# Optimization experiments

Hardware: AMD Instinct MI355X
Metric: run time of the kernel (lower is better)

Reference implementation:

```python
import jax, jax.numpy as jnp
import numpy as np

B, C, IMG, P, D, L, NH, DFF = 8, 2, 256, 16, 1024, 8, 16, 4096
HP = IMG // P          # 16 patches per side
N = HP * HP            # 256 patch tokens
S = N + 1              # + cls token
HD = D // NH           # 64 head dim


def _ln(x, w, b, eps=1e-5):
    mu = x.mean(-1, keepdims=True)
    var = ((x - mu) ** 2).mean(-1, keepdims=True)
    return (x - mu) * jax.lax.rsqrt(var + eps) * w + b


def _decay_mask():
    # RetNetRelPos2d(D, NH, initial_value=1, heads_range=NH): per-head log-decay
    decay = jnp.log(1.0 - 2.0 ** (-1.0 - NH * jnp.arange(NH, dtype=jnp.float32) / NH))
    idx = jnp.arange(HP)
    gy, gx = jnp.meshgrid(idx, idx, indexing='ij')
    grid = jnp.stack([gy.ravel(), gx.ravel()], -1)                 # [N,2]
    dist = jnp.abs(grid[:, None] - grid[None, :]).sum(-1)          # [N,N] Manhattan
    mask = decay[:, None, None] * dist.astype(jnp.float32)        # [NH,N,N]
    return jnp.pad(mask, ((0, 0), (1, 0), (1, 0)))                 # cls: zero decay


def setup_inputs() -> dict:
    key = jax.random.key(0)
    ks = iter(jax.random.split(key, 16))
    g = lambda shape: jax.random.normal(next(ks), shape, jnp.float32) * 0.02
    return dict(
        imgs=jax.random.normal(next(ks), (B, C, IMG, IMG), jnp.float32),
        patch_w=g((C, P, P, D)), patch_b=jnp.zeros((D,), jnp.float32),
        cls_tok=g((1, 1, D)),
        ln1_w=jnp.ones((L, D), jnp.float32), ln1_b=jnp.zeros((L, D), jnp.float32),
        wq=g((L, D, D)), wk=g((L, D, D)), wv=g((L, D, D)),
        bq=jnp.zeros((L, D), jnp.float32), bk=jnp.zeros((L, D), jnp.float32), bv=jnp.zeros((L, D), jnp.float32),
        wo=g((L, D, D)), bo=jnp.zeros((L, D), jnp.float32),
        ln2_w=jnp.ones((L, D), jnp.float32), ln2_b=jnp.zeros((L, D), jnp.float32),
        w1=g((L, D, DFF)), b1=jnp.zeros((L, DFF), jnp.float32),
        w2=g((L, DFF, D)), b2=jnp.zeros((L, D), jnp.float32),
        normf_w=jnp.ones((D,), jnp.float32), normf_b=jnp.zeros((D,), jnp.float32),
        enpred_w=g((D, P * P * 2)), enpred_b=jnp.zeros((P * P * 2,), jnp.float32),
    )


def reference(imgs, patch_w, patch_b, cls_tok, ln1_w, ln1_b, wq, wk, wv, bq, bk, bv,
              wo, bo, ln2_w, ln2_b, w1, b1, w2, b2, normf_w, normf_b, enpred_w, enpred_b):
    b = imgs.shape[0]
    # PatchEmbed: conv with stride==kernel == patch extraction + linear
    xp = imgs.reshape(b, C, HP, P, HP, P)
    x = jnp.einsum('nchpwq,cpqd->nhwd', xp, patch_w).reshape(b, N, D) + patch_b
    residual = x
    x = jnp.concatenate([jnp.broadcast_to(cls_tok, (b, 1, D)), x], axis=1)  # [b,S,D]
    mask = _decay_mask()  # [NH,S,S]
    scale = HD ** -0.5
    for i in range(L):  # RMT blocks: pre-LN MaSA (softmax(qk*scale + decay)) + pre-LN GELU MLP
        h = _ln(x, ln1_w[i], ln1_b[i])
        q = (h @ wq[i] + bq[i]).reshape(b, S, NH, HD)
        k = (h @ wk[i] + bk[i]).reshape(b, S, NH, HD)
        v = (h @ wv[i] + bv[i]).reshape(b, S, NH, HD)
        logits = jnp.einsum('bqhd,bkhd->bhqk', q, k) * scale + mask
        attn = jax.nn.softmax(logits, axis=-1)
        o = jnp.einsum('bhqk,bkhd->bqhd', attn, v).reshape(b, S, D)
        x = x + o @ wo[i] + bo[i]
        h = _ln(x, ln2_w[i], ln2_b[i])
        x = x + jax.nn.gelu(h @ w1[i] + b1[i], approximate=False) @ w2[i] + b2[i]
    x = _ln(x, normf_w, normf_b)
    # PGSA on patch tokens as [b,D,HP,HP]
    t = x[:, 1:, :].transpose(0, 2, 1).reshape(b, D, HP, HP)
    n = HP * HP - 1
    mu = t.mean(axis=(2, 3), keepdims=True)
    xm2 = (t - mu) ** 2
    y = xm2 / (4.0 * (xm2.sum(axis=(2, 3), keepdims=True) / n + 1e-4)) + 0.5
    t = t * jax.nn.sigmoid(y)
    tokens = t.reshape(b, D, N).transpose(0, 2, 1) + residual
    pred = tokens @ enpred_w + enpred_b  # [b,N,P*P*2]
    # unpatchify -> [b,2,IMG,IMG]
    u = pred.reshape(b, HP, HP, P, P, 2)
    return jnp.einsum('nhwpqc->nchpwq', u).reshape(b, 2, IMG, IMG)
```

## Files before the change

### kernel.cpp

```cpp
#include <hip/hip_runtime.h>
#include <cstdint>
#include <cstddef>

#define BB    8
#define CCH   2
#define IMGD  256
#define PDIM  16
#define DD    1024
#define LLAY  8
#define NHEAD 16
#define DFFD  4096
#define NTOK  256
#define SD    257
#define HDD   64
#define MTOK  (BB*SD)
#define MPAT  (BB*NTOK)
#define MPAD  2176
#define KPAD  288

typedef unsigned short u16;
typedef __bf16 bf16x8 __attribute__((ext_vector_type(8)));
typedef float  f32x4  __attribute__((ext_vector_type(4)));

__device__ __forceinline__ u16 f2bf(float f) {
    uint32_t u = __float_as_uint(f);
    u += 0x7FFF + ((u >> 16) & 1);
    return (u16)(u >> 16);
}
__device__ __forceinline__ int imin(int a, int b) { return a < b ? a : b; }

#define GLB(p)  ((const __attribute__((address_space(1))) void*)(uintptr_t)(p))
#define LDSP(p) ((__attribute__((address_space(3))) void*)(uint32_t)(uintptr_t)(p))

template<int ACT, int OBF>
__global__ __launch_bounds__(256) void gemm128(
    const u16* __restrict__ A, const u16* __restrict__ BT,
    const float* __restrict__ bias, const float* __restrict__ Cin,
    void* __restrict__ Cout, int M, int N, int K)
{
    __shared__ u16 lds[8192];
    const int tid = threadIdx.x, wid = tid >> 6, lane = tid & 63;
    const int m0 = blockIdx.y * 128, n0 = blockIdx.x * 128;
    const int wm = (wid >> 1) * 64, wn = (wid & 1) * 64;
    const int srow = lane >> 2, scol = (lane & 3) * 8;
    const int l15 = lane & 15, loct = lane >> 4;

    f32x4 acc[4][4] = {};

    const size_t arow = (size_t)(m0 + wid * 16 + srow) * K + scol;
    const size_t brow = (size_t)(n0 + wid * 16 + srow) * K + scol;
    u16* ldsA = lds + wid * 512;
    u16* ldsB = lds + 4096 + wid * 512;

    for (int k0 = 0; k0 < K; k0 += 32) {
        __builtin_amdgcn_global_load_lds(GLB(A  + arow + k0),                 LDSP(ldsA),        16, 0, 0);
        __builtin_amdgcn_global_load_lds(GLB(A  + arow + (size_t)64*K + k0),  LDSP(ldsA + 2048), 16, 0, 0);
        __builtin_amdgcn_global_load_lds(GLB(BT + brow + k0),                 LDSP(ldsB),        16, 0, 0);
        __builtin_amdgcn_global_load_lds(GLB(BT + brow + (size_t)64*K + k0),  LDSP(ldsB + 2048), 16, 0, 0);
        __syncthreads();
        bf16x8 af[4], bfr[4];
        #pragma unroll
        for (int i = 0; i < 4; ++i)
            af[i] = *(const bf16x8*)(lds + (wm + i * 16 + l15) * 32 + loct * 8);
        #pragma unroll
        for (int j = 0; j < 4; ++j)
            bfr[j] = *(const bf16x8*)(lds + 4096 + (wn + j * 16 + l15) * 32 + loct * 8);
        #pragma unroll
        for (int i = 0; i < 4; ++i)
            #pragma unroll
            for (int j = 0; j < 4; ++j)
                acc[i][j] = __builtin_amdgcn_mfma_f32_16x16x32_bf16(af[i], bfr[j], acc[i][j], 0, 0, 0);
        __syncthreads();
    }

    #pragma unroll
    for (int j = 0; j < 4; ++j) {
        const int col = n0 + wn + j * 16 + l15;
        const float bv = bias[col];
        #pragma unroll
        for (int i = 0; i < 4; ++i) {
            const int rbase = m0 + wm + i * 16 + loct * 4;
            #pragma unroll
            for (int r = 0; r < 4; ++r) {
                const int row = rbase + r;
                if (row < M) {
                    float v = acc[i][j][r] + bv;
                    if (ACT) v = 0.5f * v * (1.f + erff(v * 0.70710678118654752f));
                    if (Cin) v += Cin[(size_t)row * N + col];
                    if (OBF) ((u16*)Cout)[(size_t)row * N + col] = f2bf(v);
                    else     ((float*)Cout)[(size_t)row * N + col] = v;
                }
            }
        }
    }
}

template<int SPLIT>
__global__ __launch_bounds__(256) void gemm128_sk(
    const u16* __restrict__ A, const u16* __restrict__ BT,
    const float* __restrict__ bias, float* __restrict__ C,
    int M, int N, int K)
{
    __shared__ u16 lds[8192];
    const int tid = threadIdx.x, wid = tid >> 6, lane = tid & 63;
    const int m0 = blockIdx.y * 128, n0 = blockIdx.x * 128;
    const int wm = (wid >> 1) * 64, wn = (wid & 1) * 64;
    const int srow = lane >> 2, scol = (lane & 3) * 8;
    const int l15 = lane & 15, loct = lane >> 4;
    const int Ks = K / SPLIT;
    const int kb = blockIdx.z * Ks;

    f32x4 acc[4][4] = {};

    const size_t arow = (size_t)(m0 + wid * 16 + srow) * K + scol + kb;
    const size_t brow = (size_t)(n0 + wid * 16 + srow) * K + scol + kb;
    u16* ldsA = lds + wid * 512;
    u16* ldsB = lds + 4096 + wid * 512;

    for (int k0 = 0; k0 < Ks; k0 += 32) {
        __builtin_amdgcn_global_load_lds(GLB(A  + arow + k0),                 LDSP(ldsA),        16, 0, 0);
        __builtin_amdgcn_global_load_lds(GLB(A  + arow + (size_t)64*K + k0),  LDSP(ldsA + 2048), 16, 0, 0);
        __builtin_amdgcn_global_load_lds(GLB(BT + brow + k0),                 LDSP(ldsB),        16, 0, 0);
        __builtin_amdgcn_global_load_lds(GLB(BT + brow + (size_t)64*K + k0),  LDSP(ldsB + 2048), 16, 0, 0);
        __syncthreads();
        bf16x8 af[4], bfr[4];
        #pragma unroll
        for (int i = 0; i < 4; ++i)
            af[i] = *(const bf16x8*)(lds + (wm + i * 16 + l15) * 32 + loct * 8);
        #pragma unroll
        for (int j = 0; j < 4; ++j)
            bfr[j] = *(const bf16x8*)(lds + 4096 + (wn + j * 16 + l15) * 32 + loct * 8);
        #pragma unroll
        for (int i = 0; i < 4; ++i)
            #pragma unroll
            for (int j = 0; j < 4; ++j)
                acc[i][j] = __builtin_amdgcn_mfma_f32_16x16x32_bf16(af[i], bfr[j], acc[i][j], 0, 0, 0);
        __syncthreads();
    }

    const int z0 = (blockIdx.z == 0);
    #pragma unroll
    for (int j = 0; j < 4; ++j) {
        const int col = n0 + wn + j * 16 + l15;
        const float bv = z0 ? bias[col] : 0.f;
        #pragma unroll
        for (int i = 0; i < 4; ++i) {
            const int rbase = m0 + wm + i * 16 + loct * 4;
            #pragma unroll
            for (int r = 0; r < 4; ++r) {
                const int row = rbase + r;
                if (row < M)
                    unsafeAtomicAdd(&C[(size_t)row * N + col], acc[i][j][r] + bv);
            }
        }
    }
}

__global__ __launch_bounds__(256) void gemm_qkv(
    const u16* __restrict__ A, const u16* __restrict__ BT,
    const float* __restrict__ bq, const float* __restrict__ bk,
    const float* __restrict__ bvp,
    u16* __restrict__ QKb, u16* __restrict__ VTg, int M, int K)
{
    __shared__ u16 lds[8192];
    const int tid = threadIdx.x, wid = tid >> 6, lane = tid & 63;
    const int m0 = blockIdx.y * 128, n0 = blockIdx.x * 128;
    const int wm = (wid >> 1) * 64, wn = (wid & 1) * 64;
    const int srow = lane >> 2, scol = (lane & 3) * 8;
    const int l15 = lane & 15, loct = lane >> 4;

    f32x4 acc[4][4] = {};
    const size_t arow = (size_t)(m0 + wid * 16 + srow) * K + scol;
    const size_t brow = (size_t)(n0 + wid * 16 + srow) * K + scol;
    u16* ldsA = lds + wid * 512;
    u16* ldsB = lds + 4096 + wid * 512;

    for (int k0 = 0; k0 < K; k0 += 32) {
        __builtin_amdgcn_global_load_lds(GLB(A  + arow + k0),                 LDSP(ldsA),        16, 0, 0);
        __builtin_amdgcn_global_load_lds(GLB(A  + arow + (size_t)64*K + k0),  LDSP(ldsA + 2048), 16, 0, 0);
        __builtin_amdgcn_global_load_lds(GLB(BT + brow + k0),                 LDSP(ldsB),        16, 0, 0);
        __builtin_amdgcn_global_load_lds(GLB(BT + brow + (size_t)64*K + k0),  LDSP(ldsB + 2048), 16, 0, 0);
        __syncthreads();
        bf16x8 af[4], bfr[4];
        #pragma unroll
        for (int i = 0; i < 4; ++i)
            af[i] = *(const bf16x8*)(lds + (wm + i * 16 + l15) * 32 + loct * 8);
        #pragma unroll
        for (int j = 0; j < 4; ++j)
            bfr[j] = *(const bf16x8*)(lds + 4096 + (wn + j * 16 + l15) * 32 + loct * 8);
        #pragma unroll
        for (int i = 0; i < 4; ++i)
            #pragma unroll
            for (int j = 0; j < 4; ++j)
                acc[i][j] = __builtin_amdgcn_mfma_f32_16x16x32_bf16(af[i], bfr[j], acc[i][j], 0, 0, 0);
        __syncthreads();
    }

    #pragma unroll
    for (int j = 0; j < 4; ++j) {
        const int col = n0 + wn + j * 16 + l15;
        const float bval = (col < 1024) ? bq[col]
                         : (col < 2048) ? bk[col - 1024]
                                        : bvp[col - 2048];
        #pragma unroll
        for (int i = 0; i < 4; ++i) {
            const int rbase = m0 + wm + i * 16 + loct * 4;
            #pragma unroll
            for (int r = 0; r < 4; ++r) {
                const int row = rbase + r;
                if (row < M) {
                    const float v = acc[i][j][r] + bval;
                    if (col < 2048) {
                        QKb[(size_t)row * 2048 + col] = f2bf(v);
                    } else {
                        const int b = row / SD;
                        const int key = row - b * SD;
                        VTg[((size_t)b * 1024 + (col - 2048)) * KPAD + key] = f2bf(v);
                    }
                }
            }
        }
    }
}

template<int ACT, int OBF>
__global__ __launch_bounds__(256) void gemm64(
    const u16* __restrict__ A, const u16* __restrict__ BT,
    const float* __restrict__ bias, const float* __restrict__ Cin,
    void* __restrict__ Cout, int M, int N, int K)
{
    __shared__ u16 lds[8192];
    const int tid = threadIdx.x, wid = tid >> 6, lane = tid & 63;
    const int m0 = blockIdx.y * 64, n0 = blockIdx.x * 64;
    const int wm = (wid >> 1) * 32, wn = (wid & 1) * 32;
    const int srow = lane >> 2, scol = (lane & 3) * 8;
    const int l15 = lane & 15, loct = lane >> 4;

    f32x4 acc[2][2] = {};
    const size_t arow = (size_t)(m0 + wid * 16 + srow) * K + scol;
    const size_t brow = (size_t)(n0 + wid * 16 + srow) * K + scol;
    u16* ldsA = lds + wid * 512;
    u16* ldsB = lds + 4096 + wid * 512;

    for (int k0 = 0; k0 < K; k0 += 64) {
        __builtin_amdgcn_global_load_lds(GLB(A  + arow + k0),      LDSP(ldsA),        16, 0, 0);
        __builtin_amdgcn_global_load_lds(GLB(A  + arow + k0 + 32), LDSP(ldsA + 2048), 16, 0, 0);
        __builtin_amdgcn_global_load_lds(GLB(BT + brow + k0),      LDSP(ldsB),        16, 0, 0);
        __builtin_amdgcn_global_load_lds(GLB(BT + brow + k0 + 32), LDSP(ldsB + 2048), 16, 0, 0);
        __syncthreads();
        #pragma unroll
        for (int t = 0; t < 2; ++t) {
            bf16x8 af[2], bfr[2];
            #pragma unroll
            for (int i = 0; i < 2; ++i)
                af[i] = *(const bf16x8*)(lds + t * 2048 + (wm + i * 16 + l15) * 32 + loct * 8);
            #pragma unroll
            for (int j = 0; j < 2; ++j)
                bfr[j] = *(const bf16x8*)(lds + 4096 + t * 2048 + (wn + j * 16 + l15) * 32 + loct * 8);
            #pragma unroll
            for (int i = 0; i < 2; ++i)
                #pragma unroll
                for (int j = 0; j < 2; ++j)
                    acc[i][j] = __builtin_amdgcn_mfma_f32_16x16x32_bf16(af[i], bfr[j], acc[i][j], 0, 0, 0);
        }
        __syncthreads();
    }

    #pragma unroll
    for (int j = 0; j < 2; ++j) {
        const int col = n0 + wn + j * 16 + l15;
        const float bv = bias[col];
        #pragma unroll
        for (int i = 0; i < 2; ++i) {
            const int rbase = m0 + wm + i * 16 + loct * 4;
            #pragma unroll
            for (int r = 0; r < 4; ++r) {
                const int row = rbase + r;
                if (row < M) {
                    float v = acc[i][j][r] + bv;
                    if (ACT) v = 0.5f * v * (1.f + erff(v * 0.70710678118654752f));
                    if (Cin) v += Cin[(size_t)row * N + col];
                    if (OBF) ((u16*)Cout)[(size_t)row * N + col] = f2bf(v);
                    else     ((float*)Cout)[(size_t)row * N + col] = v;
                }
            }
        }
    }
}

__global__ __launch_bounds__(256) void attn_fused(
    const u16* __restrict__ QKb, const u16* __restrict__ VTg,
    u16* __restrict__ O)
{
    __shared__ u16 P[4][16][296];
    const int tid = threadIdx.x, wid = tid >> 6, lane = tid & 63;
    const int l15 = lane & 15, loct = lane >> 4;
    const int bh = blockIdx.x, b = bh >> 4, h = bh & 15;
    const int q0 = blockIdx.y * 64 + wid * 16;

    const size_t qkbase = (size_t)b * SD * 2048 + h * 64;
    const u16* qp = QKb + qkbase + (size_t)imin(q0 + l15, SD - 1) * 2048;
    const bf16x8 qf0 = *(const bf16x8*)(qp + loct * 8);
    const bf16x8 qf1 = *(const bf16x8*)(qp + 32 + loct * 8);

    f32x4 s[17];
    #pragma unroll
    for (int nt = 0; nt < 17; ++nt) {
        const u16* kp = QKb + qkbase + (size_t)imin(nt * 16 + l15, SD - 1) * 2048 + 1024;
        const bf16x8 kf0 = *(const bf16x8*)(kp + loct * 8);
        const bf16x8 kf1 = *(const bf16x8*)(kp + 32 + loct * 8);
        f32x4 a = {};
        a = __builtin_amdgcn_mfma_f32_16x16x32_bf16(qf0, kf0, a, 0, 0, 0);
        a = __builtin_amdgcn_mfma_f32_16x16x32_bf16(qf1, kf1, a, 0, 0, 0);
        s[nt] = a;
    }

    const float dec = logf(1.f - exp2f(-1.f - (float)h));
    const int qb = q0 + loct * 4;
    float rmax[4] = {-3.4e38f, -3.4e38f, -3.4e38f, -3.4e38f};
    #pragma unroll
    for (int nt = 0; nt < 17; ++nt) {
        const int key = nt * 16 + l15;
        #pragma unroll
        for (int r = 0; r < 4; ++r) {
            float v;
            if (key >= SD) {
                v = -1e30f;
            } else {
                v = s[nt][r] * 0.125f;
                const int q = qb + r;
                if (q > 0 && key > 0) {
                    const int nq = q - 1, nk = key - 1;
                    const int dist = abs((nq >> 4) - (nk >> 4)) + abs((nq & 15) - (nk & 15));
                    v += dec * (float)dist;
                }
            }
            s[nt][r] = v;
            rmax[r] = fmaxf(rmax[r], v);
        }
    }
    #pragma unroll
    for (int r = 0; r < 4; ++r) {
        #pragma unroll
        for (int m = 1; m < 16; m <<= 1) rmax[r] = fmaxf(rmax[r], __shfl_xor(rmax[r], m));
    }
    float rsum[4] = {0.f, 0.f, 0.f, 0.f};
    #pragma unroll
    for (int nt = 0; nt < 17; ++nt)
        #pragma unroll
        for (int r = 0; r < 4; ++r) {
            const float e = __expf(s[nt][r] - rmax[r]);
            s[nt][r] = e;
            rsum[r] += e;
        }
    #pragma unroll
    for (int r = 0; r < 4; ++r) {
        #pragma unroll
        for (int m = 1; m < 16; m <<= 1) rsum[r] += __shfl_xor(rsum[r], m);
        rsum[r] = 1.f / rsum[r];
    }
    #pragma unroll
    for (int nt = 0; nt < 17; ++nt)
        #pragma unroll
        for (int r = 0; r < 4; ++r)
            P[wid][loct * 4 + r][nt * 16 + l15] = f2bf(s[nt][r] * rsum[r]);
    {
        const int rr = lane >> 2, cc = (lane & 3) * 4;
        #pragma unroll
        for (int i = 0; i < 4; ++i) P[wid][rr][272 + cc + i] = 0;
    }

    f32x4 o[4] = {};
    const u16* vrow = VTg + ((size_t)b * 1024 + h * 64) * KPAD;
    #pragma unroll
    for (int ks = 0; ks < 9; ++ks) {
        const bf16x8 pf = *(const bf16x8*)&P[wid][l15][ks * 32 + loct * 8];
        #pragma unroll
        for (int j = 0; j < 4; ++j) {
            const bf16x8 vf = *(const bf16x8*)(vrow + (size_t)(j * 16 + l15) * KPAD + ks * 32 + loct * 8);
            o[j] = __builtin_amdgcn_mfma_f32_16x16x32_bf16(pf, vf, o[j], 0, 0, 0);
        }
    }
    #pragma unroll
    for (int j = 0; j < 4; ++j)
        #pragma unroll
        for (int r = 0; r < 4; ++r) {
            const int q = qb + r;
            if (q < SD) O[((size_t)(b * SD + q)) * DD + h * 64 + j * 16 + l15] = f2bf(o[j][r]);
        }
}

__global__ __launch_bounds__(256) void transpose_bf16_b(
    const float* __restrict__ W, u16* __restrict__ WT, int K, int N,
    size_t sstrideZ, size_t dstrideZ)
{
    __shared__ float t[32][33];
    const float* Wz = W + (size_t)blockIdx.z * sstrideZ;
    u16* WTz = WT + (size_t)blockIdx.z * dstrideZ;
    const int k0 = blockIdx.y * 32, n0 = blockIdx.x * 32;
    const int c = threadIdx.x & 31, rb = threadIdx.x >> 5;
    #pragma unroll
    for (int i = 0; i < 4; ++i) {
        const int r = rb + i * 8;
        t[r][c] = Wz[(size_t)(k0 + r) * N + n0 + c];
    }
    __syncthreads();
    #pragma unroll
    for (int i = 0; i < 4; ++i) {
        const int r = rb + i * 8;
        WTz[(size_t)(n0 + r) * K + k0 + c] = f2bf(t[c][r]);
    }
}

__global__ __launch_bounds__(256) void im2col_k(const float* __restrict__ imgs,
                                                u16* __restrict__ Ao)
{
    const int idx = blockIdx.x * 256 + threadIdx.x;
    const int k = idx & 511, m = idx >> 9;
    const int b = m >> 8, n = m & 255;
    const int hp = n >> 4, wp = n & 15;
    const int c = k >> 8, p = (k >> 4) & 15, q = k & 15;
    Ao[idx] = f2bf(imgs[(((size_t)b * CCH + c) * IMGD + hp * PDIM + p) * IMGD + wp * PDIM + q]);
}

__global__ __launch_bounds__(256) void build_x_k(const float* __restrict__ RES,
                                                 const float* __restrict__ cls,
                                                 float* __restrict__ X)
{
    const int idx = blockIdx.x * 256 + threadIdx.x;
    const int d = idx & 1023;
    const int r = idx >> 10;
    const int b = r / SD;
    const int s = r - b * SD;
    X[idx] = (s == 0) ? cls[d] : RES[((size_t)(b * NTOK + s - 1)) * DD + d];
}

template<int OBF>
__global__ __launch_bounds__(256) void ln_rows(const float* __restrict__ X,
                                               const float* __restrict__ w,
                                               const float* __restrict__ bsrc,
                                               void* __restrict__ Y)
{
    const int row = blockIdx.x;
    const int tid = threadIdx.x;
    const float* xr = X + (size_t)row * DD;
    const float4 v = *(const float4*)(xr + tid * 4);
    float s  = v.x + v.y + v.z + v.w;
    float s2 = v.x * v.x + v.y * v.y + v.z * v.z + v.w * v.w;
    #pragma unroll
    for (int off = 1; off < 64; off <<= 1) {
        s  += __shfl_xor(s, off);
        s2 += __shfl_xor(s2, off);
    }
    __shared__ float rs[4], rs2[4];
    if ((tid & 63) == 0) { rs[tid >> 6] = s; rs2[tid >> 6] = s2; }
    __syncthreads();
    s  = rs[0] + rs[1] + rs[2] + rs[3];
    s2 = rs2[0] + rs2[1] + rs2[2] + rs2[3];
    const float mu  = s * (1.f / 1024.f);
    const float var = fmaf(-mu, mu, s2 * (1.f / 1024.f));
    const float ri  = rsqrtf(var + 1e-5f);
    const float4 wv = *(const float4*)(w + tid * 4);
    const float4 bv = *(const float4*)(bsrc + tid * 4);
    float4 o;
    o.x = (v.x - mu) * ri * wv.x + bv.x;
    o.y = (v.y - mu) * ri * wv.y + bv.y;
    o.z = (v.z - mu) * ri * wv.z + bv.z;
    o.w = (v.w - mu) * ri * wv.w + bv.w;
    if (OBF) {
        ushort4 o4 = make_ushort4(f2bf(o.x), f2bf(o.y), f2bf(o.z), f2bf(o.w));
        *(ushort4*)((u16*)Y + (size_t)row * DD + tid * 4) = o4;
    } else {
        *(float4*)((float*)Y + (size_t)row * DD + tid * 4) = o;
    }
}

__global__ __launch_bounds__(256) void pgsa_k(const float* __restrict__ Xf,
                                              const float* __restrict__ RES,
                                              u16* __restrict__ TOK)
{
    const int bd = blockIdx.x;
    const int b = bd >> 10, dch = bd & 1023;
    const int n = threadIdx.x;
    const float t = Xf[((size_t)(b * SD + 1 + n)) * DD + dch];
    __shared__ float red[4];
    float s = t;
    #pragma unroll
    for (int off = 1; off < 64; off <<= 1) s += __shfl_xor(s, off);
    if ((n & 63) == 0) red[n >> 6] = s;
    __syncthreads();
    const float mu = (red[0] + red[1] + red[2] + red[3]) * (1.f / 256.f);
    const float xm = t - mu;
    const float xm2 = xm * xm;
    __syncthreads();
    float s2 = xm2;
    #pragma unroll
    for (int off = 1; off < 64; off <<= 1) s2 += __shfl_xor(s2, off);
    if ((n & 63) == 0) red[n >> 6] = s2;
    __syncthreads();
    const float tot2 = red[0] + red[1] + red[2] + red[3];
    const float y = xm2 / (4.f * (tot2 * (1.f / 255.f) + 1e-4f)) + 0.5f;
    const float sig = 1.f / (1.f + expf(-y));
    const size_t ri = ((size_t)b * NTOK + n) * DD + dch;
    TOK[ri] = f2bf(fmaf(t, sig, RES[ri]));
}

__global__ __launch_bounds__(256) void unpatch_k(const float* __restrict__ PRED,
                                                 float* __restrict__ out)
{
    const int idx = blockIdx.x * 256 + threadIdx.x;
    const int j = idx & 255, i = (idx >> 8) & 255;
    const int c = (idx >> 16) & 1, b = idx >> 17;
    const int hp = i >> 4, p = i & 15, wp = j >> 4, q = j & 15;
    out[idx] = PRED[((size_t)b * NTOK + hp * 16 + wp) * 512 + (p * 16 + q) * 2 + c];
}

extern "C" void kernel_launch(void* const* d_in, const int* in_sizes, int n_in,
                              void* d_out, int out_size, void* d_ws, size_t ws_size,
                              hipStream_t stream)
{
    const float* imgs     = (const float*)d_in[0];
    const float* patch_w  = (const float*)d_in[1];
    const float* patch_b  = (const float*)d_in[2];
    const float* cls_tok  = (const float*)d_in[3];
    const float* ln1_w    = (const float*)d_in[4];
    const float* ln1_b    = (const float*)d_in[5];
    const float* wq       = (const float*)d_in[6];
    const float* wk       = (const float*)d_in[7];
    const float* wv       = (const float*)d_in[8];
    const float* bq       = (const float*)d_in[9];
    const float* bk       = (const float*)d_in[10];
    const float* bv       = (const float*)d_in[11];
    const float* wo       = (const float*)d_in[12];
    const float* bo       = (const float*)d_in[13];
    const float* ln2_w    = (const float*)d_in[14];
    const float* ln2_b    = (const float*)d_in[15];
    const float* w1       = (const float*)d_in[16];
    const float* b1       = (const float*)d_in[17];
    const float* w2       = (const float*)d_in[18];
    const float* b2       = (const float*)d_in[19];
    const float* normf_w  = (const float*)d_in[20];
    const float* normf_b  = (const float*)d_in[21];
    const float* enpred_w = (const float*)d_in[22];
    const float* enpred_b = (const float*)d_in[23];
    float* out = (float*)d_out;

    char* w = (char*)d_ws;
    float* X     = (float*)w;            w += (size_t)MTOK * DD * 4;
    float* RES   = (float*)w;            w += (size_t)MPAT * DD * 4;
    u16*   QKb   = (u16*)w;              w += (size_t)MPAD * 2048 * 2;
    u16*   VTg   = (u16*)w;              w += (size_t)BB * 1024 * KPAD * 2;
    char*  UNION = w;                    w += (size_t)MPAD * DFFD * 2;
    u16*   Hb    = (u16*)w;              w += (size_t)MPAD * DD * 2;
    u16*   Ob    = (u16*)w;              w += (size_t)MPAD * DD * 2;
    u16*   WTqkv = (u16*)w;              w += (size_t)LLAY * 3072 * DD * 2;
    u16*   WTwo  = (u16*)w;              w += (size_t)LLAY * DD * DD * 2;
    u16*   WTw1  = (u16*)w;              w += (size_t)LLAY * DFFD * DD * 2;
    u16*   WTw2  = (u16*)w;              w += (size_t)LLAY * DD * DFFD * 2;
    u16*   WTpe  = (u16*)w;              w += (size_t)DD * 512 * 2;
    u16*   WTen  = (u16*)w;              w += (size_t)512 * DD * 2;

    u16*   IM2b  = (u16*)UNION;
    u16*   GELUb = (u16*)UNION;
    float* PRED  = (float*)UNION;
    float* Hf    = (float*)QKb;
    u16*   TOKb  = Hb;

    hipMemsetAsync(VTg, 0, (size_t)BB * 1024 * KPAD * 2, stream);

    hipLaunchKernelGGL(transpose_bf16_b, dim3(DD / 32, 512 / 32, 1), dim3(256), 0, stream,
                       patch_w, WTpe, 512, DD, 0, 0);
    hipLaunchKernelGGL(transpose_bf16_b, dim3(32, 32, LLAY), dim3(256), 0, stream,
                       wq, WTqkv,                     DD, DD, (size_t)DD * DD, (size_t)3072 * DD);
    hipLaunchKernelGGL(transpose_bf16_b, dim3(32, 32, LLAY), dim3(256), 0, stream,
                       wk, WTqkv + (size_t)1024 * DD, DD, DD, (size_t)DD * DD, (size_t)3072 * DD);
    hipLaunchKernelGGL(transpose_bf16_b, dim3(32, 32, LLAY), dim3(256), 0, stream,
                       wv, WTqkv + (size_t)2048 * DD, DD, DD, (size_t)DD * DD, (size_t)3072 * DD);
    hipLaunchKernelGGL(transpose_bf16_b, dim3(32, 32, LLAY), dim3(256), 0, stream,
                       wo, WTwo, DD, DD, (size_t)DD * DD, (size_t)DD * DD);
    hipLaunchKernelGGL(transpose_bf16_b, dim3(DFFD / 32, DD / 32, LLAY), dim3(256), 0, stream,
                       w1, WTw1, DD, DFFD, (size_t)DD * DFFD, (size_t)DFFD * DD);
    hipLaunchKernelGGL(transpose_bf16_b, dim3(DD / 32, DFFD / 32, LLAY), dim3(256), 0, stream,
                       w2, WTw2, DFFD, DD, (size_t)DFFD * DD, (size_t)DD * DFFD);
    hipLaunchKernelGGL(transpose_bf16_b, dim3(512 / 32, DD / 32, 1), dim3(256), 0, stream,
                       enpred_w, WTen, DD, 512, 0, 0);

    hipLaunchKernelGGL(im2col_k, dim3(4096), dim3(256), 0, stream, imgs, IM2b);
    hipLaunchKernelGGL((gemm64<0,0>), dim3(DD / 64, MPAT / 64), dim3(256), 0, stream,
                       IM2b, WTpe, patch_b, (const float*)nullptr, (void*)RES, MPAT, DD, 512);
    hipLaunchKernelGGL(build_x_k, dim3(MTOK * DD / 256), dim3(256), 0, stream, RES, cls_tok, X);

    for (int i = 0; i < LLAY; ++i) {
        hipLaunchKernelGGL((ln_rows<1>), dim3(MTOK), dim3(256), 0, stream,
                           X, ln1_w + i * DD, ln1_b + i * DD, (void*)Hb);
        hipLaunchKernelGGL(gemm_qkv, dim3(3072 / 128, 17), dim3(256), 0, stream,
                           Hb, WTqkv + (size_t)i * 3072 * DD,
                           bq + i * DD, bk + i * DD, bv + i * DD, QKb, VTg, MTOK, DD);
        hipLaunchKernelGGL(attn_fused, dim3(BB * NHEAD, 5), dim3(256), 0, stream,
                           QKb, VTg, Ob);
        hipLaunchKernelGGL((gemm64<0,0>), dim3(DD / 64, 33), dim3(256), 0, stream,
                           Ob, WTwo + (size_t)i * DD * DD, bo + i * DD, X, (void*)X, MTOK, DD, DD);
        hipLaunchKernelGGL((ln_rows<1>), dim3(MTOK), dim3(256), 0, stream,
                           X, ln2_w + i * DD, ln2_b + i * DD, (void*)Hb);
        hipLaunchKernelGGL((gemm128<1,1>), dim3(DFFD / 128, 17), dim3(256), 0, stream,
                           Hb, WTw1 + (size_t)i * DFFD * DD, b1 + i * DFFD,
                           (const float*)nullptr, (void*)GELUb, MTOK, DFFD, DD);
        hipLaunchKernelGGL((gemm128_sk<4>), dim3(DD / 128, 17, 4), dim3(256), 0, stream,
                           GELUb, WTw2 + (size_t)i * DD * DFFD, b2 + i * DD, X, MTOK, DD, DFFD);
    }

    hipLaunchKernelGGL((ln_rows<0>), dim3(MTOK), dim3(256), 0, stream, X, normf_w, normf_b, (void*)Hf);
    hipLaunchKernelGGL(pgsa_k, dim3(BB * DD), dim3(256), 0, stream, Hf, RES, TOKb);
    hipLaunchKernelGGL((gemm64<0,0>), dim3(512 / 64, MPAT / 64), dim3(256), 0, stream,
                       TOKb, WTen, enpred_b, (const float*)nullptr, (void*)PRED, MPAT, 512, DD);
    hipLaunchKernelGGL(unpatch_k, dim3(4096), dim3(256), 0, stream, PRED, out);
}
```

Baseline: 2.184 ms.

## Overlap per-layer weight transposes with GEMM blocks and rework MLP/LN kernels

Weight transpose-to-bf16 work for each layer now runs as extra blocks inside the patch-embed GEMM and inside the previous layer's MLP1 GEMM launch, instead of as separate up-front launches. The goal is to hide that conversion cost behind compute and cut launch count. The split-K atomic MLP2 GEMM is replaced by the gemm64 kernel with a residual add. LayerNorm now handles one row per wavefront without block syncs, and the transpose tile grows to 64x64. The risks are extra LDS use, mixed-workload blocks causing imbalance, and losing the split-K parallelism.

New measurement: 1.942 ms. 11.1% less time.

```diff
diff --git a/kernel.cpp b/kernel.cpp
--- a/kernel.cpp
+++ b/kernel.cpp
@@ -32,13 +32,64 @@
 #define GLB(p)  ((const __attribute__((address_space(1))) void*)(uintptr_t)(p))
 #define LDSP(p) ((__attribute__((address_space(3))) void*)(uint32_t)(uintptr_t)(p))
 
-template<int ACT, int OBF>
-__global__ __launch_bounds__(256) void gemm128(
+__device__ __forceinline__ void tp64(const float* __restrict__ W,
+                                     u16* __restrict__ WT, int K, int N,
+                                     int k0, int n0, float (*t)[65])
+{
+    const int c = threadIdx.x & 63, r4 = threadIdx.x >> 6;
+    #pragma unroll
+    for (int i = 0; i < 16; ++i) {
+        const int r = i * 4 + r4;
+        t[r][c] = W[(size_t)(k0 + r) * N + n0 + c];
+    }
+    __syncthreads();
+    #pragma unroll
+    for (int i = 0; i < 16; ++i) {
+        const int r = i * 4 + r4;
+        WT[(size_t)(n0 + r) * K + k0 + c] = f2bf(t[c][r]);
+    }
+}
+
+__device__ __forceinline__ void tp_dispatch(
+    int t, const float* wqN, const float* wkN, const float* wvN,
+    const float* woN, const float* w1N, const float* w2N,
+    u16* WTqkvN, u16* WTwoN, u16* WTw1N, u16* WTw2N, float (*tb)[65])
+{
+    if (t < 768) {
+        const int which = t >> 8, local = t & 255;
+        const float* W = which == 0 ? wqN : which == 1 ? wkN : wvN;
+        tp64(W, WTqkvN + (size_t)which * 1024 * DD, DD, DD,
+             (local >> 4) * 64, (local & 15) * 64, tb);
+    } else if (t < 1024) {
+        const int local = t - 768;
+        tp64(woN, WTwoN, DD, DD, (local >> 4) * 64, (local & 15) * 64, tb);
+    } else if (t < 2048) {
+        const int local = t - 1024;
+        tp64(w1N, WTw1N, DD, DFFD, (local >> 6) * 64, (local & 63) * 64, tb);
+    } else {
+        const int local = t - 2048;
+        tp64(w2N, WTw2N, DFFD, DD, (local >> 4) * 64, (local & 15) * 64, tb);
+    }
+}
+
+__global__ __launch_bounds__(256) void mlp1_tp(
     const u16* __restrict__ A, const u16* __restrict__ BT,
-    const float* __restrict__ bias, const float* __restrict__ Cin,
-    void* __restrict__ Cout, int M, int N, int K)
-{
-    __shared__ u16 lds[8192];
+    const float* __restrict__ bias, u16* __restrict__ Cout, int M,
+    const float* __restrict__ wqN, const float* __restrict__ wkN,
+    const float* __restrict__ wvN, const float* __restrict__ woN,
+    const float* __restrict__ w1N, const float* __restrict__ w2N,
+    u16* __restrict__ WTqkvN, u16* __restrict__ WTwoN,
+    u16* __restrict__ WTw1N, u16* __restrict__ WTw2N)
+{
+    __shared__ float smem[64 * 65];
+    if (blockIdx.y >= 17) {
+        const int t = (blockIdx.y - 17) * 32 + blockIdx.x;
+        tp_dispatch(t, wqN, wkN, wvN, woN, w1N, w2N,
+                    WTqkvN, WTwoN, WTw1N, WTw2N, (float(*)[65])smem);
+        return;
+    }
+    u16* lds = (u16*)smem;
+    const int N = DFFD, K = DD;
     const int tid = threadIdx.x, wid = tid >> 6, lane = tid & 63;
     const int m0 = blockIdx.y * 128, n0 = blockIdx.x * 128;
     const int wm = (wid >> 1) * 64, wn = (wid & 1) * 64;
@@ -46,7 +97,6 @@
     const int l15 = lane & 15, loct = lane >> 4;
 
     f32x4 acc[4][4] = {};
-
     const size_t arow = (size_t)(m0 + wid * 16 + srow) * K + scol;
     const size_t brow = (size_t)(n0 + wid * 16 + srow) * K + scol;
     u16* ldsA = lds + wid * 512;
@@ -85,72 +135,79 @@
                 const int row = rbase + r;
                 if (row < M) {
                     float v = acc[i][j][r] + bv;
-                    if (ACT) v = 0.5f * v * (1.f + erff(v * 0.70710678118654752f));
-                    if (Cin) v += Cin[(size_t)row * N + col];
-                    if (OBF) ((u16*)Cout)[(size_t)row * N + col] = f2bf(v);
-                    else     ((float*)Cout)[(size_t)row * N + col] = v;
+                    v = 0.5f * v * (1.f + erff(v * 0.70710678118654752f));
+                    Cout[(size_t)row * N + col] = f2bf(v);
                 }
             }
         }
     }
 }
 
-template<int SPLIT>
-__global__ __launch_bounds__(256) void gemm128_sk(
+__global__ __launch_bounds__(256) void patch_tp(
     const u16* __restrict__ A, const u16* __restrict__ BT,
-    const float* __restrict__ bias, float* __restrict__ C,
-    int M, int N, int K)
-{
-    __shared__ u16 lds[8192];
+    const float* __restrict__ bias, float* __restrict__ Cout,
+    const float* __restrict__ wq0, const float* __restrict__ wk0,
+    const float* __restrict__ wv0, const float* __restrict__ wo0,
+    const float* __restrict__ w10, const float* __restrict__ w20,
+    u16* __restrict__ WTqkv0, u16* __restrict__ WTwo0,
+    u16* __restrict__ WTw10, u16* __restrict__ WTw20)
+{
+    __shared__ float smem[64 * 65];
+    if (blockIdx.y >= 32) {
+        const int t = (blockIdx.y - 32) * 16 + blockIdx.x;
+        tp_dispatch(t, wq0, wk0, wv0, wo0, w10, w20,
+                    WTqkv0, WTwo0, WTw10, WTw20, (float(*)[65])smem);
+        return;
+    }
+    u16* lds = (u16*)smem;
+    const int N = DD, K = 512;
     const int tid = threadIdx.x, wid = tid >> 6, lane = tid & 63;
-    const int m0 = blockIdx.y * 128, n0 = blockIdx.x * 128;
-    const int wm = (wid >> 1) * 64, wn = (wid & 1) * 64;
+    const int m0 = blockIdx.y * 64, n0 = blockIdx.x * 64;
+    const int wm = (wid >> 1) * 32, wn = (wid & 1) * 32;
     const int srow = lane >> 2, scol = (lane & 3) * 8;
     const int l15 = lane & 15, loct = lane >> 4;
-    const int Ks = K / SPLIT;
-    const int kb = blockIdx.z * Ks;
-
-    f32x4 acc[4][4] = {};
-
-    const size_t arow = (size_t)(m0 + wid * 16 + srow) * K + scol + kb;
-    const size_t brow = (size_t)(n0 + wid * 16 + srow) * K + scol + kb;
+
+    f32x4 acc[2][2] = {};
+    const size_t arow = (size_t)(m0 + wid * 16 + srow) * K + scol;
+    const size_t brow = (size_t)(n0 + wid * 16 + srow) * K + scol;
     u16* ldsA = lds + wid * 512;
     u16* ldsB = lds + 4096 + wid * 512;
 
-    for (int k0 = 0; k0 < Ks; k0 += 32) {
-        __builtin_amdgcn_global_load_lds(GLB(A  + arow + k0),                 LDSP(ldsA),        16, 0, 0);
-        __builtin_amdgcn_global_load_lds(GLB(A  + arow + (size_t)64*K + k0),  LDSP(ldsA + 2048), 16, 0, 0);
-        __builtin_amdgcn_global_load_lds(GLB(BT + brow + k0),                 LDSP(ldsB),        16, 0, 0);
-        __builtin_amdgcn_global_load_lds(GLB(BT + brow + (size_t)64*K + k0),  LDSP(ldsB + 2048), 16, 0, 0);
-        __syncthreads();
-        bf16x8 af[4], bfr[4];
-        #pragma unroll
-        for (int i = 0; i < 4; ++i)
-            af[i] = *(const bf16x8*)(lds + (wm + i * 16 + l15) * 32 + loct * 8);
-        #pragma unroll
-        for (int j = 0; j < 4; ++j)
-            bfr[j] = *(const bf16x8*)(lds + 4096 + (wn + j * 16 + l15) * 32 + loct * 8);
-        #pragma unroll
-        for (int i = 0; i < 4; ++i)
-            #pragma unroll
-            for (int j = 0; j < 4; ++j)
-                acc[i][j] = __builtin_amdgcn_mfma_f32_16x16x32_bf16(af[i], bfr[j], acc[i][j], 0, 0, 0);
-        __syncthreads();
-    }
-
-    const int z0 = (blockIdx.z == 0);
-    #pragma unroll
-    for (int j = 0; j < 4; ++j) {
+    for (int k0 = 0; k0 < K; k0 += 64) {
+        __builtin_amdgcn_global_load_lds(GLB(A  + arow + k0),      LDSP(ldsA),        16, 0, 0);
+        __builtin_amdgcn_global_load_lds(GLB(A  + arow + k0 + 32), LDSP(ldsA + 2048), 16, 0, 0);
+        __builtin_amdgcn_global_load_lds(GLB(BT + brow + k0),      LDSP(ldsB),        16, 0, 0);
+        __builtin_amdgcn_global_load_lds(GLB(BT + brow + k0 + 32), LDSP(ldsB + 2048), 16, 0, 0);
+        __syncthreads();
+        #pragma unroll
+        for (int t = 0; t < 2; ++t) {
+            bf16x8 af[2], bfr[2];
+            #pragma unroll
+            for (int i = 0; i < 2; ++i)
+                af[i] = *(const bf16x8*)(lds + t * 2048 + (wm + i * 16 + l15) * 32 + loct * 8);
+            #pragma unroll
+            for (int j = 0; j < 2; ++j)
+                bfr[j] = *(const bf16x8*)(lds + 4096 + t * 2048 + (wn + j * 16 + l15) * 32 + loct * 8);
+            #pragma unroll
+            for (int i = 0; i < 2; ++i)
+                #pragma unroll
+                for (int j = 0; j < 2; ++j)
+                    acc[i][j] = __builtin_amdgcn_mfma_f32_16x16x32_bf16(af[i], bfr[j], acc[i][j], 0, 0, 0);
+        }
+        __syncthreads();
+    }
+
+    #pragma unroll
+    for (int j = 0; j < 2; ++j) {
         const int col = n0 + wn + j * 16 + l15;
-        const float bv = z0 ? bias[col] : 0.f;
-        #pragma unroll
-        for (int i = 0; i < 4; ++i) {
+        const float bv = bias[col];
+        #pragma unroll
+        for (int i = 0; i < 2; ++i) {
             const int rbase = m0 + wm + i * 16 + loct * 4;
             #pragma unroll
             for (int r = 0; r < 4; ++r) {
                 const int row = rbase + r;
-                if (row < M)
-                    unsafeAtomicAdd(&C[(size_t)row * N + col], acc[i][j][r] + bv);
+                Cout[(size_t)row * N + col] = acc[i][j][r] + bv;
             }
         }
     }
@@ -394,22 +451,9 @@
     const float* __restrict__ W, u16* __restrict__ WT, int K, int N,
     size_t sstrideZ, size_t dstrideZ)
 {
-    __shared__ float t[32][33];
-    const float* Wz = W + (size_t)blockIdx.z * sstrideZ;
-    u16* WTz = WT + (size_t)blockIdx.z * dstrideZ;
-    const int k0 = blockIdx.y * 32, n0 = blockIdx.x * 32;
-    const int c = threadIdx.x & 31, rb = threadIdx.x >> 5;
-    #pragma unroll
-    for (int i = 0; i < 4; ++i) {
-        const int r = rb + i * 8;
-        t[r][c] = Wz[(size_t)(k0 + r) * N + n0 + c];
-    }
-    __syncthreads();
-    #pragma unroll
-    for (int i = 0; i < 4; ++i) {
-        const int r = rb + i * 8;
-        WTz[(size_t)(n0 + r) * K + k0 + c] = f2bf(t[c][r]);
-    }
+    __shared__ float t[64][65];
+    tp64(W + (size_t)blockIdx.z * sstrideZ, WT + (size_t)blockIdx.z * dstrideZ,
+         K, N, blockIdx.y * 64, blockIdx.x * 64, t);
 }
 
 __global__ __launch_bounds__(256) void im2col_k(const float* __restrict__ imgs,
@@ -441,37 +485,40 @@
                                                const float* __restrict__ bsrc,
                                                void* __restrict__ Y)
 {
-    const int row = blockIdx.x;
-    const int tid = threadIdx.x;
+    const int wid = threadIdx.x >> 6, lane = threadIdx.x & 63;
+    const int row = blockIdx.x * 4 + wid;
     const float* xr = X + (size_t)row * DD;
-    const float4 v = *(const float4*)(xr + tid * 4);
-    float s  = v.x + v.y + v.z + v.w;
-    float s2 = v.x * v.x + v.y * v.y + v.z * v.z + v.w * v.w;
+    float4 v[4];
+    float s = 0.f, s2 = 0.f;
+    #pragma unroll
+    for (int i = 0; i < 4; ++i) {
+        v[i] = *(const float4*)(xr + (i * 64 + lane) * 4);
+        s  += v[i].x + v[i].y + v[i].z + v[i].w;
+        s2 += v[i].x * v[i].x + v[i].y * v[i].y + v[i].z * v[i].z + v[i].w * v[i].w;
+    }
     #pragma unroll
     for (int off = 1; off < 64; off <<= 1) {
         s  += __shfl_xor(s, off);
         s2 += __shfl_xor(s2, off);
     }
-    __shared__ float rs[4], rs2[4];
-    if ((tid & 63) == 0) { rs[tid >> 6] = s; rs2[tid >> 6] = s2; }
-    __syncthreads();
-    s  = rs[0] + rs[1] + rs[2] + rs[3];
-    s2 = rs2[0] + rs2[1] + rs2[2] + rs2[3];
     const float mu  = s * (1.f / 1024.f);
     const float var = fmaf(-mu, mu, s2 * (1.f / 1024.f));
     const float ri  = rsqrtf(var + 1e-5f);
-    const float4 wv = *(const float4*)(w + tid * 4);
-    const float4 bv = *(const float4*)(bsrc + tid * 4);
-    float4 o;
-    o.x = (v.x - mu) * ri * wv.x + bv.x;
-    o.y = (v.y - mu) * ri * wv.y + bv.y;
-    o.z = (v.z - mu) * ri * wv.z + bv.z;
-    o.w = (v.w - mu) * ri * wv.w + bv.w;
-    if (OBF) {
-        ushort4 o4 = make_ushort4(f2bf(o.x), f2bf(o.y), f2bf(o.z), f2bf(o.w));
-        *(ushort4*)((u16*)Y + (size_t)row * DD + tid * 4) = o4;
-    } else {
-        *(float4*)((float*)Y + (size_t)row * DD + tid * 4) = o;
+    #pragma unroll
+    for (int i = 0; i < 4; ++i) {
+        const float4 wv = *(const float4*)(w + (i * 64 + lane) * 4);
+        const float4 bv = *(const float4*)(bsrc + (i * 64 + lane) * 4);
+        float4 o;
+        o.x = (v[i].x - mu) * ri * wv.x + bv.x;
+        o.y = (v[i].y - mu) * ri * wv.y + bv.y;
+        o.z = (v[i].z - mu) * ri * wv.z + bv.z;
+        o.w = (v[i].w - mu) * ri * wv.w + bv.w;
+        if (OBF) {
+            ushort4 o4 = make_ushort4(f2bf(o.x), f2bf(o.y), f2bf(o.z), f2bf(o.w));
+            *(ushort4*)((u16*)Y + (size_t)row * DD + (i * 64 + lane) * 4) = o4;
+        } else {
+            *(float4*)((float*)Y + (size_t)row * DD + (i * 64 + lane) * 4) = o;
+        }
     }
 }
 
@@ -568,30 +615,20 @@
 
     hipMemsetAsync(VTg, 0, (size_t)BB * 1024 * KPAD * 2, stream);
 
-    hipLaunchKernelGGL(transpose_bf16_b, dim3(DD / 32, 512 / 32, 1), dim3(256), 0, stream,
-                       patch_w, WTpe, 512, DD, 0, 0);
-    hipLaunchKernelGGL(transpose_bf16_b, dim3(32, 32, LLAY), dim3(256), 0, stream,
-                       wq, WTqkv,                     DD, DD, (size_t)DD * DD, (size_t)3072 * DD);
-    hipLaunchKernelGGL(transpose_bf16_b, dim3(32, 32, LLAY), dim3(256), 0, stream,
-                       wk, WTqkv + (size_t)1024 * DD, DD, DD, (size_t)DD * DD, (size_t)3072 * DD);
-    hipLaunchKernelGGL(transpose_bf16_b, dim3(32, 32, LLAY), dim3(256), 0, stream,
-                       wv, WTqkv + (size_t)2048 * DD, DD, DD, (size_t)DD * DD, (size_t)3072 * DD);
-    hipLaunchKernelGGL(transpose_bf16_b, dim3(32, 32, LLAY), dim3(256), 0, stream,
-                       wo, WTwo, DD, DD, (size_t)DD * DD, (size_t)DD * DD);
-    hipLaunchKernelGGL(transpose_bf16_b, dim3(DFFD / 32, DD / 32, LLAY), dim3(256), 0, stream,
-                       w1, WTw1, DD, DFFD, (size_t)DD * DFFD, (size_t)DFFD * DD);
-    hipLaunchKernelGGL(transpose_bf16_b, dim3(DD / 32, DFFD / 32, LLAY), dim3(256), 0, stream,
-                       w2, WTw2, DFFD, DD, (size_t)DFFD * DD, (size_t)DD * DFFD);
-    hipLaunchKernelGGL(transpose_bf16_b, dim3(512 / 32, DD / 32, 1), dim3(256), 0, stream,
-                       enpred_w, WTen, DD, 512, 0, 0);
-
+    hipLaunchKernelGGL(transpose_bf16_b, dim3(DD / 64, 512 / 64, 1), dim3(256), 0, stream,
+                       patch_w, WTpe, 512, DD, (size_t)0, (size_t)0);
+    hipLaunchKernelGGL(transpose_bf16_b, dim3(512 / 64, DD / 64, 1), dim3(256), 0, stream,
+                       enpred_w, WTen, DD, 512, (size_t)0, (size_t)0);
     hipLaunchKernelGGL(im2col_k, dim3(4096), dim3(256), 0, stream, imgs, IM2b);
-    hipLaunchKernelGGL((gemm64<0,0>), dim3(DD / 64, MPAT / 64), dim3(256), 0, stream,
-                       IM2b, WTpe, patch_b, (const float*)nullptr, (void*)RES, MPAT, DD, 512);
+
+    hipLaunchKernelGGL(patch_tp, dim3(DD / 64, 32 + 192), dim3(256), 0, stream,
+                       IM2b, WTpe, patch_b, RES,
+                       wq, wk, wv, wo, w1, w2,
+                       WTqkv, WTwo, WTw1, WTw2);
     hipLaunchKernelGGL(build_x_k, dim3(MTOK * DD / 256), dim3(256), 0, stream, RES, cls_tok, X);
 
     for (int i = 0; i < LLAY; ++i) {
-        hipLaunchKernelGGL((ln_rows<1>), dim3(MTOK), dim3(256), 0, stream,
+        hipLaunchKernelGGL((ln_rows<1>), dim3(MTOK / 4), dim3(256), 0, stream,
                            X, ln1_w + i * DD, ln1_b + i * DD, (void*)Hb);
         hipLaunchKernelGGL(gemm_qkv, dim3(3072 / 128, 17), dim3(256), 0, stream,
                            Hb, WTqkv + (size_t)i * 3072 * DD,
@@ -600,16 +637,28 @@
                            QKb, VTg, Ob);
         hipLaunchKernelGGL((gemm64<0,0>), dim3(DD / 64, 33), dim3(256), 0, stream,
                            Ob, WTwo + (size_t)i * DD * DD, bo + i * DD, X, (void*)X, MTOK, DD, DD);
-        hipLaunchKernelGGL((ln_rows<1>), dim3(MTOK), dim3(256), 0, stream,
+        hipLaunchKernelGGL((ln_rows<1>), dim3(MTOK / 4), dim3(256), 0, stream,
                            X, ln2_w + i * DD, ln2_b + i * DD, (void*)Hb);
-        hipLaunchKernelGGL((gemm128<1,1>), dim3(DFFD / 128, 17), dim3(256), 0, stream,
-                           Hb, WTw1 + (size_t)i * DFFD * DD, b1 + i * DFFD,
-                           (const float*)nullptr, (void*)GELUb, MTOK, DFFD, DD);
-        hipLaunchKernelGGL((gemm128_sk<4>), dim3(DD / 128, 17, 4), dim3(256), 0, stream,
-                           GELUb, WTw2 + (size_t)i * DD * DFFD, b2 + i * DD, X, MTOK, DD, DFFD);
-    }
-
-    hipLaunchKernelGGL((ln_rows<0>), dim3(MTOK), dim3(256), 0, stream, X, normf_w, normf_b, (void*)Hf);
+        if (i < LLAY - 1) {
+            const size_t n1 = (size_t)(i + 1);
+            hipLaunchKernelGGL(mlp1_tp, dim3(DFFD / 128, 17 + 96), dim3(256), 0, stream,
+                               Hb, WTw1 + (size_t)i * DFFD * DD, b1 + i * DFFD, GELUb, MTOK,
+                               wq + n1 * DD * DD, wk + n1 * DD * DD, wv + n1 * DD * DD,
+                               wo + n1 * DD * DD, w1 + n1 * DD * DFFD, w2 + n1 * DFFD * DD,
+                               WTqkv + n1 * 3072 * DD, WTwo + n1 * DD * DD,
+                               WTw1 + n1 * DFFD * DD, WTw2 + n1 * DD * DFFD);
+        } else {
+            hipLaunchKernelGGL(mlp1_tp, dim3(DFFD / 128, 17), dim3(256), 0, stream,
+                               Hb, WTw1 + (size_t)i * DFFD * DD, b1 + i * DFFD, GELUb, MTOK,
+                               (const float*)nullptr, (const float*)nullptr, (const float*)nullptr,
+                               (const float*)nullptr, (const float*)nullptr, (const float*)nullptr,
+                               (u16*)nullptr, (u16*)nullptr, (u16*)nullptr, (u16*)nullptr);
+        }
+        hipLaunchKernelGGL((gemm64<0,0>), dim3(DD / 64, 33), dim3(256), 0, stream,
+                           GELUb, WTw2 + (size_t)i * DD * DFFD, b2 + i * DD, X, (void*)X, MTOK, DD, DFFD);
+    }
+
+    hipLaunchKernelGGL((ln_rows<0>), dim3(MTOK / 4), dim3(256), 0, stream, X, normf_w, normf_b, (void*)Hf);
     hipLaunchKernelGGL(pgsa_k, dim3(BB * DD), dim3(256), 0, stream, Hf, RES, TOKb);
     hipLaunchKernelGGL((gemm64<0,0>), dim3(512 / 64, MPAT / 64), dim3(256), 0, stream,
                        TOKb, WTen, enpred_b, (const float*)nullptr, (void*)PRED, MPAT, 512, DD);
```
